# Performance work log

Measured on AMD Instinct MI355X. Metric: run time of the kernel, lower is better.

Reference implementation:

```python
import jax, jax.numpy as jnp
import numpy as np

N = 100000   # nodes
E = 3200000  # directed edges
F_IN = 128   # data.num_node_features
H = 16       # hidden
C = 2        # output classes (hard-coded in module)


def _glorot(key, fan_in, fan_out):
    s = jnp.sqrt(6.0 / (fan_in + fan_out)).astype(jnp.float32)
    return jax.random.uniform(key, (fan_in, fan_out), jnp.float32, -s, s)


def setup_inputs() -> dict:
    key = jax.random.key(0)
    ks = jax.random.split(key, 5)
    x = jax.random.normal(ks[0], (N, F_IN), jnp.float32)
    edge_index = jax.random.randint(ks[1], (2, E), 0, N, dtype=jnp.int64)
    return {
        "x": x,
        "edge_index": edge_index,
        "W1": _glorot(ks[2], F_IN, H), "b1": jnp.zeros((H,), jnp.float32),
        "W2": _glorot(ks[3], H, H),    "b2": jnp.zeros((H,), jnp.float32),
        "W3": _glorot(ks[4], H, C),    "b3": jnp.zeros((C,), jnp.float32),
    }


def _gcn_conv(x, W, b, src, dst, norm, n):
    # PyG GCNConv: linear transform, then normalized gather -> scatter-add, + bias
    h = x @ W                                   # [N, out]
    msg = h[src] * norm[:, None]                # [E+N, out] gather over source nodes
    out = jax.ops.segment_sum(msg, dst, num_segments=n)  # scatter-add at targets
    return out + b


def reference(x, edge_index, W1, b1, W2, b2, W3, b3):
    n = x.shape[0]
    loop = jnp.arange(n, dtype=edge_index.dtype)
    src = jnp.concatenate([edge_index[0], loop])  # add self-loops (PyG default)
    dst = jnp.concatenate([edge_index[1], loop])
    # symmetric normalization: deg^{-1/2}[src] * deg^{-1/2}[dst], deg = in-degree w/ self-loops
    deg = jax.ops.segment_sum(jnp.ones(src.shape, jnp.float32), dst, num_segments=n)
    dis = jnp.where(deg > 0, jax.lax.rsqrt(jnp.maximum(deg, 1.0)), 0.0)
    norm = dis[src] * dis[dst]
    # dropout is identity in eval mode
    h = jax.nn.relu(_gcn_conv(x, W1, b1, src, dst, norm, n))
    h = jax.nn.relu(_gcn_conv(h, W2, b2, src, dst, norm, n))
    h = _gcn_conv(h, W3, b3, src, dst, norm, n)
    return jax.nn.log_softmax(h, axis=1)
```

## Files before the change

### kernel.cpp

```cpp
#include <hip/hip_runtime.h>
#include <math.h>

#define NSB   512
#define CB    512
#define BSH   8
#define BKN   256
#define ESMAX 6272
#define SLOT  10240

typedef _Float16 h8  __attribute__((ext_vector_type(8)));
typedef _Float16 h4  __attribute__((ext_vector_type(4)));
typedef _Float16 h2v __attribute__((ext_vector_type(2)));

__device__ inline int wave_scan_incl(int v) {
    int lane = threadIdx.x & 63;
#pragma unroll
    for (int d = 1; d < 64; d <<= 1) {
        int t = __shfl_up(v, d, 64);
        if (lane >= d) v += t;
    }
    return v;
}


__global__ __launch_bounds__(512) void k_bucket(
        const int* __restrict__ src, const int* __restrict__ dst,
        unsigned* __restrict__ col, int* __restrict__ cnt2d, int* __restrict__ ofs2d,
        int e, int es) {
    __shared__ unsigned sorted[ESMAX];
    __shared__ int lc[512], lcur[512];
    __shared__ int wsum[8];
    int tid = threadIdx.x;
    int c = blockIdx.x;
    lc[tid] = 0;
    __syncthreads();
    int lo = c * es;
    int hi = min(lo + es, e);
    for (int i = lo + tid; i < hi; i += 512)
        atomicAdd(&lc[dst[i] >> BSH], 1);
    __syncthreads();
    int cv = lc[tid];
    int inc = wave_scan_incl(cv);
    int wid = tid >> 6;
    if ((tid & 63) == 63) wsum[wid] = inc;
    __syncthreads();
    int wofs = 0;
#pragma unroll
    for (int w = 0; w < 8; w++) wofs += (w < wid) ? wsum[w] : 0;
    int excl = inc - cv + wofs;
    lcur[tid] = excl;
    cnt2d[(size_t)c * CB + tid] = cv;
    ofs2d[(size_t)c * CB + tid] = excl;
    __syncthreads();
    for (int i = lo + tid; i < hi; i += 512) {
        int d = dst[i];
        int b = d >> BSH;
        int p = atomicAdd(&lcur[b], 1);
        sorted[p] = ((unsigned)src[i] << BSH) | (unsigned)(d & (BKN - 1));
    }
    __syncthreads();
    int cnt_ = hi - lo;
    for (int i = tid; i < cnt_; i += 512)
        col[(size_t)c * es + i] = sorted[i];
}


__global__ __launch_bounds__(512) void k_sort(
        const unsigned* __restrict__ col, const int* __restrict__ cnt2d,
        const int* __restrict__ ofs2d,
        int* __restrict__ col2, int* __restrict__ rs,
        int* __restrict__ re, float* __restrict__ dis,
        int n, int nch, int es) {
    __shared__ int sdat[SLOT];
    __shared__ int cnt[BKN], cur[BKN];
    __shared__ int wsum8[8];
    __shared__ int wsum4[4];
    int tid = threadIdx.x;
    int b = blockIdx.x;
    int lo = b * SLOT;

    int nc = (tid < nch) ? cnt2d[(size_t)tid * CB + b] : 0;
    int inc = wave_scan_incl(nc);
    int wid = tid >> 6;
    if ((tid & 63) == 63) wsum8[wid] = inc;
    __syncthreads();
    int wofs = 0, tot = 0;
#pragma unroll
    for (int w = 0; w < 8; w++) {
        wofs += (w < wid) ? wsum8[w] : 0;
        tot += wsum8[w];
    }
    int base = inc - nc + wofs;
    if (tot > SLOT) tot = SLOT;
    if (base + nc > SLOT) nc = max(0, SLOT - base);
    if (tid < BKN) cnt[tid] = 0;
    if (nc > 0) {
        size_t sbase = (size_t)tid * es + ofs2d[(size_t)tid * CB + b];
        for (int k = 0; k < nc; k++)
            sdat[base + k] = (int)col[sbase + k];
    }
    __syncthreads();
    for (int i = tid; i < tot; i += 512)
        atomicAdd(&cnt[sdat[i] & (BKN - 1)], 1);
    __syncthreads();
    int c = (tid < BKN) ? cnt[tid] : 0;
    int inc2 = wave_scan_incl(c);
    if (tid < BKN && (tid & 63) == 63) wsum4[wid] = inc2;
    __syncthreads();
    if (tid < BKN) {
        int wofs2 = 0;
#pragma unroll
        for (int w = 0; w < 4; w++) wofs2 += (w < wid) ? wsum4[w] : 0;
        int excl2 = inc2 - c + wofs2;
        cur[tid] = lo + excl2;
        int node = (b << BSH) + tid;
        if (node < n) {
            rs[node] = lo + excl2;
            re[node] = lo + excl2 + c;
            dis[node] = rsqrtf((float)(c + 1));
        }
    }
    __syncthreads();
    for (int i = tid; i < tot; i += 512) {
        int v = sdat[i];
        int pos = atomicAdd(&cur[v & (BKN - 1)], 1);
        col2[pos] = v >> BSH;
    }
}


__global__ __launch_bounds__(512) void k_linear1s(
        const float* __restrict__ x, const float* __restrict__ W,
        const float* __restrict__ dis, _Float16* __restrict__ hs, int n) {
    __shared__ float sW[2048];
    int tid = threadIdx.x;
    for (int i = tid; i < 2048; i += 512) sW[i] = W[i];
    __syncthreads();
    int cg = tid & 3;
    int kg = (tid >> 2) & 7;
    int nl = tid >> 5;
    float wr[16][4];
#pragma unroll
    for (int j = 0; j < 16; j++)
#pragma unroll
        for (int cc = 0; cc < 4; cc++)
            wr[j][cc] = sW[(kg * 16 + j) * 16 + cg * 4 + cc];
    int nodeBase = blockIdx.x * 128 + nl;
    for (int it = 0; it < 8; it++) {
        int node = nodeBase + it * 16;
        float a0 = 0.f, a1 = 0.f, a2 = 0.f, a3 = 0.f;
        if (node < n) {
            const float4* xr = (const float4*)(x + (size_t)node * 128 + kg * 16);
#pragma unroll
            for (int j4 = 0; j4 < 4; j4++) {
                float4 xv = xr[j4];
                float xs0 = xv.x, xs1 = xv.y, xs2 = xv.z, xs3 = xv.w;
                int j = j4 * 4;
                a0 += xs0 * wr[j][0] + xs1 * wr[j+1][0] + xs2 * wr[j+2][0] + xs3 * wr[j+3][0];
                a1 += xs0 * wr[j][1] + xs1 * wr[j+1][1] + xs2 * wr[j+2][1] + xs3 * wr[j+3][1];
                a2 += xs0 * wr[j][2] + xs1 * wr[j+1][2] + xs2 * wr[j+2][2] + xs3 * wr[j+3][2];
                a3 += xs0 * wr[j][3] + xs1 * wr[j+1][3] + xs2 * wr[j+2][3] + xs3 * wr[j+3][3];
            }
        }
#pragma unroll
        for (int m = 4; m <= 16; m <<= 1) {
            a0 += __shfl_xor(a0, m);
            a1 += __shfl_xor(a1, m);
            a2 += __shfl_xor(a2, m);
            a3 += __shfl_xor(a3, m);
        }
        if (kg == 0 && node < n) {
            float d = dis[node];
            h4 o;
            o[0] = (_Float16)(a0 * d);
            o[1] = (_Float16)(a1 * d);
            o[2] = (_Float16)(a2 * d);
            o[3] = (_Float16)(a3 * d);
            *((h4*)(hs + (size_t)node * 16 + cg * 4)) = o;
        }
    }
}


__global__ void k_pullA(const _Float16* __restrict__ hs, const int* __restrict__ rs,
                        const int* __restrict__ re, const int* __restrict__ col2,
                        const float* __restrict__ dis, const float* __restrict__ bb,
                        const float* __restrict__ W, _Float16* __restrict__ hsOut, int n) {
    __shared__ float sW[256];
    __shared__ float sb[16];
    if (threadIdx.x < 256) sW[threadIdx.x] = W[threadIdx.x];
    if (threadIdx.x < 16) sb[threadIdx.x] = bb[threadIdx.x];
    __syncthreads();
    long long t = (long long)blockIdx.x * blockDim.x + threadIdx.x;
    int node = (int)(t >> 3), sub = (int)(t & 7);
    int q = sub & 1, qt = sub >> 1;
    if (node >= n) return;
    const h8* H = (const h8*)hs;
    float acc[8];
    if (qt == 0) {
        h8 self = H[(size_t)node * 2 + q];
#pragma unroll
        for (int j = 0; j < 8; j++) acc[j] = (float)self[j];
    } else {
#pragma unroll
        for (int j = 0; j < 8; j++) acc[j] = 0.f;
    }
    int b = rs[node], e2 = re[node];
    int i = b + qt;
    for (; i + 12 < e2; i += 16) {
        int s0 = col2[i], s1 = col2[i + 4], s2 = col2[i + 8], s3 = col2[i + 12];
        h8 v0 = H[(size_t)s0 * 2 + q];
        h8 v1 = H[(size_t)s1 * 2 + q];
        h8 v2 = H[(size_t)s2 * 2 + q];
        h8 v3 = H[(size_t)s3 * 2 + q];
#pragma unroll
        for (int j = 0; j < 8; j++)
            acc[j] += (float)v0[j] + (float)v1[j] + (float)v2[j] + (float)v3[j];
    }
    for (; i < e2; i += 4) {
        h8 v = H[(size_t)col2[i] * 2 + q];
#pragma unroll
        for (int j = 0; j < 8; j++) acc[j] += (float)v[j];
    }
#pragma unroll
    for (int j = 0; j < 8; j++) {
        acc[j] += __shfl_xor(acc[j], 2);
        acc[j] += __shfl_xor(acc[j], 4);
    }
    float d = dis[node];
    float va[16];
#pragma unroll
    for (int j = 0; j < 8; j++) {
        int k = q * 8 + j;
        float v = acc[j] * d + sb[k];
        v = v > 0.f ? v : 0.f;
        float other = __shfl_xor(v, 1);
        va[j]     = q ? other : v;
        va[8 + j] = q ? v : other;
    }
    if (qt == 0) {
        h8 o;
#pragma unroll
        for (int j = 0; j < 8; j++) {
            int c = q * 8 + j;
            float s = 0.f;
#pragma unroll
            for (int k = 0; k < 16; k++) s += va[k] * sW[k * 16 + c];
            o[j] = (_Float16)(s * d);
        }
        ((h8*)hsOut)[(size_t)node * 2 + q] = o;
    }
}


__global__ void k_pullB(const _Float16* __restrict__ hs, const int* __restrict__ rs,
                        const int* __restrict__ re, const int* __restrict__ col2,
                        const float* __restrict__ dis, const float* __restrict__ bb,
                        const float* __restrict__ W, _Float16* __restrict__ hs2, int n) {
    __shared__ float sW[32];
    __shared__ float sb[16];
    if (threadIdx.x < 32) sW[threadIdx.x] = W[threadIdx.x];
    if (threadIdx.x < 16) sb[threadIdx.x] = bb[threadIdx.x];
    __syncthreads();
    long long t = (long long)blockIdx.x * blockDim.x + threadIdx.x;
    int node = (int)(t >> 3), sub = (int)(t & 7);
    int q = sub & 1, qt = sub >> 1;
    if (node >= n) return;
    const h8* H = (const h8*)hs;
    float acc[8];
    if (qt == 0) {
        h8 self = H[(size_t)node * 2 + q];
#pragma unroll
        for (int j = 0; j < 8; j++) acc[j] = (float)self[j];
    } else {
#pragma unroll
        for (int j = 0; j < 8; j++) acc[j] = 0.f;
    }
    int b = rs[node], e2 = re[node];
    int i = b + qt;
    for (; i + 12 < e2; i += 16) {
        int s0 = col2[i], s1 = col2[i + 4], s2 = col2[i + 8], s3 = col2[i + 12];
        h8 v0 = H[(size_t)s0 * 2 + q];
        h8 v1 = H[(size_t)s1 * 2 + q];
        h8 v2 = H[(size_t)s2 * 2 + q];
        h8 v3 = H[(size_t)s3 * 2 + q];
#pragma unroll
        for (int j = 0; j < 8; j++)
            acc[j] += (float)v0[j] + (float)v1[j] + (float)v2[j] + (float)v3[j];
    }
    for (; i < e2; i += 4) {
        h8 v = H[(size_t)col2[i] * 2 + q];
#pragma unroll
        for (int j = 0; j < 8; j++) acc[j] += (float)v[j];
    }
#pragma unroll
    for (int j = 0; j < 8; j++) {
        acc[j] += __shfl_xor(acc[j], 2);
        acc[j] += __shfl_xor(acc[j], 4);
    }
    float d = dis[node];
    float p0 = 0.f, p1 = 0.f;
#pragma unroll
    for (int j = 0; j < 8; j++) {
        int k = q * 8 + j;
        float v = acc[j] * d + sb[k];
        v = v > 0.f ? v : 0.f;
        p0 += v * sW[k * 2 + 0];
        p1 += v * sW[k * 2 + 1];
    }
    p0 += __shfl_xor(p0, 1);
    p1 += __shfl_xor(p1, 1);
    if (sub == 0) {
        h2v o;
        o[0] = (_Float16)(p0 * d);
        o[1] = (_Float16)(p1 * d);
        ((h2v*)hs2)[node] = o;
    }
}


__global__ void k_pull2lsm(const _Float16* __restrict__ hs2, const int* __restrict__ rs,
                           const int* __restrict__ re, const int* __restrict__ col2,
                           const float* __restrict__ dis, const float* __restrict__ b3,
                           float* __restrict__ out, int n) {
    long long t = (long long)blockIdx.x * blockDim.x + threadIdx.x;
    int node = (int)(t >> 2), qt = (int)(t & 3);
    if (node >= n) return;
    const h2v* H = (const h2v*)hs2;
    float a0 = 0.f, a1 = 0.f;
    if (qt == 0) {
        h2v self = H[node];
        a0 = (float)self[0]; a1 = (float)self[1];
    }
    int b = rs[node], e2 = re[node];
    int i = b + qt;
    for (; i + 12 < e2; i += 16) {
        h2v v0 = H[col2[i]];
        h2v v1 = H[col2[i + 4]];
        h2v v2 = H[col2[i + 8]];
        h2v v3 = H[col2[i + 12]];
        a0 += (float)v0[0] + (float)v1[0] + (float)v2[0] + (float)v3[0];
        a1 += (float)v0[1] + (float)v1[1] + (float)v2[1] + (float)v3[1];
    }
    for (; i < e2; i += 4) {
        h2v v = H[col2[i]];
        a0 += (float)v[0];
        a1 += (float)v[1];
    }
    a0 += __shfl_xor(a0, 1); a0 += __shfl_xor(a0, 2);
    a1 += __shfl_xor(a1, 1); a1 += __shfl_xor(a1, 2);
    if (qt == 0) {
        float d = dis[node];
        float z0 = a0 * d + b3[0];
        float z1 = a1 * d + b3[1];
        float m = fmaxf(z0, z1);
        float l = m + logf(expf(z0 - m) + expf(z1 - m));
        float2 o = {z0 - l, z1 - l};
        ((float2*)out)[node] = o;
    }
}


extern "C" void kernel_launch(void* const* d_in, const int* in_sizes, int n_in,
                              void* d_out, int out_size, void* d_ws, size_t ws_size,
                              hipStream_t stream) {
    const float* x  = (const float*)d_in[0];
    const int*   ei = (const int*)d_in[1];
    const float* W1 = (const float*)d_in[2];
    const float* b1 = (const float*)d_in[3];
    const float* W2 = (const float*)d_in[4];
    const float* b2 = (const float*)d_in[5];
    const float* W3 = (const float*)d_in[6];
    const float* b3 = (const float*)d_in[7];
    float* out = (float*)d_out;

    const int N = in_sizes[0] / 128;
    const int E = in_sizes[1] / 2;
    const int* src = ei;
    const int* dst = ei + E;

    const int NBUCK = (N + BKN - 1) >> BSH;
    const int ES = (E + NSB - 1) / NSB;

    char* ws = (char*)d_ws;
    size_t off = 0;
    auto alloc = [&](size_t bytes) {
        void* p = ws + off;
        off += (bytes + 255) & ~(size_t)255;
        return p;
    };
    unsigned*  col   = (unsigned*)alloc((size_t)NSB * ES * sizeof(unsigned));
    int*       cnt2d = (int*)alloc((size_t)NSB * CB * sizeof(int));
    int*       ofs2d = (int*)alloc((size_t)NSB * CB * sizeof(int));
    int*       col2  = (int*)alloc((size_t)NBUCK * SLOT * sizeof(int));
    int*       rs    = (int*)alloc((size_t)N * sizeof(int));
    int*       re    = (int*)alloc((size_t)N * sizeof(int));
    float*     dis   = (float*)alloc((size_t)N * sizeof(float));
    _Float16*  hsA   = (_Float16*)alloc((size_t)N * 16 * sizeof(_Float16));
    _Float16*  hsB   = (_Float16*)alloc((size_t)N * 16 * sizeof(_Float16));
    _Float16*  hs2   = (_Float16*)alloc((size_t)N * 2 * sizeof(_Float16));

    const int B = 256;
    auto g = [&](long long work) { return (int)((work + B - 1) / B); };

    k_bucket<<<NSB, 512, 0, stream>>>(src, dst, col, cnt2d, ofs2d, E, ES);

    k_sort<<<NBUCK, 512, 0, stream>>>(col, cnt2d, ofs2d, col2, rs, re, dis, N, NSB, ES);

    k_linear1s<<<(N + 127) / 128, 512, 0, stream>>>(x, W1, dis, hsA, N);

    k_pullA<<<g((long long)N * 8), B, 0, stream>>>(hsA, rs, re, col2, dis, b1, W2, hsB, N);

    k_pullB<<<g((long long)N * 8), B, 0, stream>>>(hsB, rs, re, col2, dis, b2, W3, hs2, N);

    k_pull2lsm<<<g((long long)N * 4), B, 0, stream>>>(hs2, rs, re, col2, dis, b3, out, N);
}
```

Before: 237.0 us.

## Double bucket-sort chunks and vectorize edge loads and stores

Doubles the number of edge chunks in the bucketing pass to 1024, halving each chunk's shared-memory buffer so more blocks can be resident. Edge src/dst reads and the write of the sorted chunk now use 128-bit int4/uint4 accesses, with the chunk size padded to a multiple of 4. The per-bucket gather kernel now scans chunk counts in two halves of 512 to cover the larger chunk count. The trade-offs are more count/offset metadata to read and an extra barrier round in the gather kernel. Clamping ES to ESMAX could drop edges for larger graphs.

```diff
diff --git a/kernel.cpp b/kernel.cpp
--- a/kernel.cpp
+++ b/kernel.cpp
@@ -1,11 +1,11 @@
 #include <hip/hip_runtime.h>
 #include <math.h>
 
-#define NSB   512
+#define NSB   1024
 #define CB    512
 #define BSH   8
 #define BKN   256
-#define ESMAX 6272
+#define ESMAX 3200
 #define SLOT  10240
 
 typedef _Float16 h8  __attribute__((ext_vector_type(8)));
@@ -27,7 +27,7 @@
         const int* __restrict__ src, const int* __restrict__ dst,
         unsigned* __restrict__ col, int* __restrict__ cnt2d, int* __restrict__ ofs2d,
         int e, int es) {
-    __shared__ unsigned sorted[ESMAX];
+    __shared__ __align__(16) unsigned sorted[ESMAX];
     __shared__ int lc[512], lcur[512];
     __shared__ int wsum[8];
     int tid = threadIdx.x;
@@ -36,8 +36,19 @@
     __syncthreads();
     int lo = c * es;
     int hi = min(lo + es, e);
-    for (int i = lo + tid; i < hi; i += 512)
-        atomicAdd(&lc[dst[i] >> BSH], 1);
+    int cnt_ = hi - lo;
+    int nv = cnt_ >> 2;
+    const int4* d4 = (const int4*)(dst + lo);
+    const int4* s4 = (const int4*)(src + lo);
+    for (int i = tid; i < nv; i += 512) {
+        int4 d = d4[i];
+        atomicAdd(&lc[d.x >> BSH], 1);
+        atomicAdd(&lc[d.y >> BSH], 1);
+        atomicAdd(&lc[d.z >> BSH], 1);
+        atomicAdd(&lc[d.w >> BSH], 1);
+    }
+    for (int i = (nv << 2) + tid; i < cnt_; i += 512)
+        atomicAdd(&lc[dst[lo + i] >> BSH], 1);
     __syncthreads();
     int cv = lc[tid];
     int inc = wave_scan_incl(cv);
@@ -52,15 +63,29 @@
     cnt2d[(size_t)c * CB + tid] = cv;
     ofs2d[(size_t)c * CB + tid] = excl;
     __syncthreads();
-    for (int i = lo + tid; i < hi; i += 512) {
-        int d = dst[i];
-        int b = d >> BSH;
-        int p = atomicAdd(&lcur[b], 1);
-        sorted[p] = ((unsigned)src[i] << BSH) | (unsigned)(d & (BKN - 1));
-    }
-    __syncthreads();
-    int cnt_ = hi - lo;
-    for (int i = tid; i < cnt_; i += 512)
+    for (int i = tid; i < nv; i += 512) {
+        int4 d = d4[i];
+        int4 s = s4[i];
+        int p;
+        p = atomicAdd(&lcur[d.x >> BSH], 1);
+        sorted[p] = ((unsigned)s.x << BSH) | (unsigned)(d.x & (BKN - 1));
+        p = atomicAdd(&lcur[d.y >> BSH], 1);
+        sorted[p] = ((unsigned)s.y << BSH) | (unsigned)(d.y & (BKN - 1));
+        p = atomicAdd(&lcur[d.z >> BSH], 1);
+        sorted[p] = ((unsigned)s.z << BSH) | (unsigned)(d.z & (BKN - 1));
+        p = atomicAdd(&lcur[d.w >> BSH], 1);
+        sorted[p] = ((unsigned)s.w << BSH) | (unsigned)(d.w & (BKN - 1));
+    }
+    for (int i = (nv << 2) + tid; i < cnt_; i += 512) {
+        int d = dst[lo + i];
+        int p = atomicAdd(&lcur[d >> BSH], 1);
+        sorted[p] = ((unsigned)src[lo + i] << BSH) | (unsigned)(d & (BKN - 1));
+    }
+    __syncthreads();
+    uint4* co4 = (uint4*)(col + (size_t)c * es);
+    const uint4* so4 = (const uint4*)sorted;
+    for (int i = tid; i < nv; i += 512) co4[i] = so4[i];
+    for (int i = (nv << 2) + tid; i < cnt_; i += 512)
         col[(size_t)c * es + i] = sorted[i];
 }
 
@@ -78,28 +103,33 @@
     int tid = threadIdx.x;
     int b = blockIdx.x;
     int lo = b * SLOT;
-
-    int nc = (tid < nch) ? cnt2d[(size_t)tid * CB + b] : 0;
-    int inc = wave_scan_incl(nc);
     int wid = tid >> 6;
-    if ((tid & 63) == 63) wsum8[wid] = inc;
-    __syncthreads();
-    int wofs = 0, tot = 0;
-#pragma unroll
-    for (int w = 0; w < 8; w++) {
-        wofs += (w < wid) ? wsum8[w] : 0;
-        tot += wsum8[w];
-    }
-    int base = inc - nc + wofs;
-    if (tot > SLOT) tot = SLOT;
-    if (base + nc > SLOT) nc = max(0, SLOT - base);
     if (tid < BKN) cnt[tid] = 0;
-    if (nc > 0) {
-        size_t sbase = (size_t)tid * es + ofs2d[(size_t)tid * CB + b];
-        for (int k = 0; k < nc; k++)
-            sdat[base + k] = (int)col[sbase + k];
-    }
-    __syncthreads();
+
+    int tot = 0;
+    for (int h = 0; h < 2; h++) {
+        int ch = h * 512 + tid;
+        int nc = (ch < nch) ? cnt2d[(size_t)ch * CB + b] : 0;
+        int inc = wave_scan_incl(nc);
+        if ((tid & 63) == 63) wsum8[wid] = inc;
+        __syncthreads();
+        int wofs = 0, half = 0;
+#pragma unroll
+        for (int w = 0; w < 8; w++) {
+            wofs += (w < wid) ? wsum8[w] : 0;
+            half += wsum8[w];
+        }
+        int base = tot + inc - nc + wofs;
+        if (base + nc > SLOT) nc = max(0, SLOT - base);
+        if (nc > 0) {
+            size_t sbase = (size_t)ch * es + ofs2d[(size_t)ch * CB + b];
+            for (int k = 0; k < nc; k++)
+                sdat[base + k] = (int)col[sbase + k];
+        }
+        tot += half;
+        if (tot > SLOT) tot = SLOT;
+        __syncthreads();
+    }
     for (int i = tid; i < tot; i += 512)
         atomicAdd(&cnt[sdat[i] & (BKN - 1)], 1);
     __syncthreads();
@@ -380,7 +410,9 @@
     const int* dst = ei + E;
 
     const int NBUCK = (N + BKN - 1) >> BSH;
-    const int ES = (E + NSB - 1) / NSB;
+    int ES = (E + NSB - 1) / NSB;
+    ES = (ES + 3) & ~3;
+    if (ES > ESMAX) ES = ESMAX;
 
     char* ws = (char*)d_ws;
     size_t off = 0;
```

Measured after the change: 236.5 us. No clear change (-0.2%).
